# Kernel optimization log

Hardware: AMD Instinct MI355X
Metric: run time of the kernel (lower is better)

## Reference

```python
import jax, jax.numpy as jnp
import numpy as np
from jax import lax

B, T_ENCO, N_INP, N_HID, T_DECO = 1024, 128, 128, 256, 24


def _lin(x, W, b):
    return x @ W.T + b


def _lstm_cell(x, h, c, Wih, Whh, bih, bhh):
    # PyTorch LSTMCell gate order: input, forget, cell(g), output
    g = x @ Wih.T + bih + h @ Whh.T + bhh
    i, f, gg, o = jnp.split(g, 4, axis=-1)
    c2 = jax.nn.sigmoid(f) * c + jax.nn.sigmoid(i) * jnp.tanh(gg)
    return jax.nn.sigmoid(o) * jnp.tanh(c2), c2


def setup_inputs() -> dict:
    key = jax.random.key(0)
    ks = iter(jax.random.split(key, 48))
    def w(shape, s=0.05):
        return jax.random.normal(next(ks), shape, jnp.float32) * s
    m = N_HID
    return {
        "input_p_q": jax.random.normal(next(ks), (B, T_ENCO, N_INP), jnp.float32),
        "label_p": jax.random.normal(next(ks), (B, T_DECO), jnp.float32),
        "Ue_W": w((m, T_ENCO)), "Ue_b": w((m,)),
        "Ue2_W": w((m, N_INP)), "Ue2_b": w((m,)),
        "We_W": w((m, 2 * N_HID)), "We_b": w((m,)),
        "Ve_W": w((1, m)), "Ve_b": w((1,)),
        "Ud_W": w((N_HID, N_HID)), "Ud_b": w((N_HID,)),
        "Wd_W": w((N_HID, 2 * N_HID)), "Wd_b": w((N_HID,)),
        "Vd_W": w((1, N_HID)), "Vd_b": w((1,)),
        "enc_Wih": w((4 * N_HID, N_INP)), "enc_Whh": w((4 * N_HID, N_HID)),
        "enc_bih": w((4 * N_HID,)), "enc_bhh": w((4 * N_HID,)),
        "mid_Wih": w((4 * N_HID, N_HID)), "mid_Whh": w((4 * N_HID, N_HID)),
        "mid_bih": w((4 * N_HID,)), "mid_bhh": w((4 * N_HID,)),
        "dec_Wih": w((4 * N_HID, N_HID)), "dec_Whh": w((4 * N_HID, N_HID)),
        "dec_bih": w((4 * N_HID,)), "dec_bhh": w((4 * N_HID,)),
        "reg_W": w((1, N_HID)), "reg_b": w((1,)),
    }


def reference(input_p_q, label_p, Ue_W, Ue_b, Ue2_W, Ue2_b, We_W, We_b, Ve_W, Ve_b,
              Ud_W, Ud_b, Wd_W, Wd_b, Vd_W, Vd_b,
              enc_Wih, enc_Whh, enc_bih, enc_bhh,
              mid_Wih, mid_Whh, mid_bih, mid_bhh,
              dec_Wih, dec_Whh, dec_bih, dec_bhh,
              reg_W, reg_b):
    bsz = input_p_q.shape[0]
    inputs = input_p_q[:, :T_ENCO, :]                       # [B, T, n_inp]
    # Ue(inputs.transpose(1,2)) is loop-invariant: [B, n_inp, m]
    ue_x = _lin(jnp.swapaxes(inputs, 1, 2), Ue_W, Ue_b)
    z = jnp.zeros((bsz, N_HID), inputs.dtype)

    # --- spatial-attention encoder (LSTMCell over time) ---
    def enc_step(carry, x_i):                               # x_i: [B, n_inp]
        h, c = carry
        hc = _lin(jnp.concatenate([h, c], axis=1), We_W, We_b)[:, None, :]
        xi = _lin(x_i, Ue2_W, Ue2_b)[:, None, :]
        score = _lin(jnp.tanh(hc + ue_x + xi), Ve_W, Ve_b)[..., 0]  # [B, n_inp]
        a = jax.nn.softmax(score, axis=1)
        h2, c2 = _lstm_cell(x_i * a, h, c, enc_Wih, enc_Whh, enc_bih, enc_bhh)
        return (h2, c2), h2

    _, enc_hs = lax.scan(enc_step, (z, z), jnp.swapaxes(inputs, 0, 1))  # [T, B, H]

    # --- middle single-layer LSTM (zero init state) ---
    def mid_step(carry, x_t):
        h, c = carry
        h2, c2 = _lstm_cell(x_t, h, c, mid_Wih, mid_Whh, mid_bih, mid_bhh)
        return (h2, c2), h2

    _, mid = lax.scan(mid_step, (z, z), enc_hs)
    mid = jnp.swapaxes(mid, 0, 1)                            # [B, T, H]
    ud_mid = _lin(mid, Ud_W, Ud_b)                           # loop-invariant

    # --- temporal-attention decoder (note: raw (un-softmaxed) scores used in bmm,
    #     matching the original code) ---
    def dec_step(carry, _):
        hi, ci = carry
        wd = _lin(jnp.concatenate([hi, ci], axis=1), Wd_W, Wd_b)[:, None, :]
        t = _lin(jnp.tanh(wd + ud_mid), Vd_W, Vd_b)[..., 0]  # [B, T]
        dec_in = jnp.einsum('bt,bth->bh', t, mid)
        hi2, ci2 = _lstm_cell(dec_in, hi, ci, dec_Wih, dec_Whh, dec_bih, dec_bhh)
        return (hi2, ci2), hi2

    _, dec = lax.scan(dec_step, (z, z), None, length=T_DECO + 6)
    dec = jnp.swapaxes(dec, 0, 1)                            # [B, T_deco+6, H]
    out = _lin(dec, reg_W, reg_b)[..., 0]                    # [B, T_deco+6]
    return out[:, -T_DECO:]
```

## Files before the change

kernel.cpp:

```cpp
#include <hip/hip_runtime.h>


#define B_   1024
#define T_   128
#define NI_  128
#define H_   256
#define H4_  1024
#define TD_  24
#define DS_  30
#define BB   4
#define TB   1024

typedef _Float16 hf_t;
typedef _Float16 half8  __attribute__((ext_vector_type(8)));
typedef _Float16 half2v __attribute__((ext_vector_type(2)));

__device__ __forceinline__ float sigm(float x) {
    return __builtin_amdgcn_rcpf(1.0f + __expf(-x));
}
__device__ __forceinline__ float tanh_f(float x) {
    float e = __expf(2.0f * x);
    return 1.0f - 2.0f * __builtin_amdgcn_rcpf(e + 1.0f);
}
__device__ __forceinline__ float fdot2f(half2v a, half2v b, float c) {
#if __has_builtin(__builtin_amdgcn_fdot2)
    return __builtin_amdgcn_fdot2(a, b, c, false);
#else
    return fmaf((float)a.x, (float)b.x, fmaf((float)a.y, (float)b.y, c));
#endif
}
__device__ __forceinline__ float dot8h(half8 w, half8 x, float acc) {
    acc = fdot2f(__builtin_shufflevector(w, w, 0, 1), __builtin_shufflevector(x, x, 0, 1), acc);
    acc = fdot2f(__builtin_shufflevector(w, w, 2, 3), __builtin_shufflevector(x, x, 2, 3), acc);
    acc = fdot2f(__builtin_shufflevector(w, w, 4, 5), __builtin_shufflevector(x, x, 4, 5), acc);
    acc = fdot2f(__builtin_shufflevector(w, w, 6, 7), __builtin_shufflevector(x, x, 6, 7), acc);
    return acc;
}
__device__ __forceinline__ hf_t nt_load_h(const hf_t* p) {
#if __has_builtin(__builtin_nontemporal_load)
    return __builtin_nontemporal_load(p);
#else
    return *p;
#endif
}
__device__ __forceinline__ void nt_store_h(hf_t v, hf_t* p) {
#if __has_builtin(__builtin_nontemporal_store)
    __builtin_nontemporal_store(v, p);
#else
    *p = v;
#endif
}

#define W_WE    0u
#define W_UE2   131072u
#define W_EWIH  163840u
#define W_EWHH  294912u
#define W_MWIH  557056u
#define W_MWHH  819200u
#define W_DWIH  1081344u
#define W_DWHH  1343488u
#define W_WD    1605632u
#define W_UD    1736704u
#define SCR_A   2097152u
#define SCR_B   35651584u

__global__ void convw_kernel(const float* __restrict__ sWE, const float* __restrict__ sUE2,
                             const float* __restrict__ sEI, const float* __restrict__ sEH,
                             const float* __restrict__ sMI, const float* __restrict__ sMH,
                             const float* __restrict__ sDI, const float* __restrict__ sDH,
                             const float* __restrict__ sWD, const float* __restrict__ sUD,
                             hf_t* __restrict__ dst) {
    const int gtid = blockIdx.x * blockDim.x + threadIdx.x;
    const int gs   = gridDim.x * blockDim.x;
    for (int n = gtid; n < 131072; n += gs) {
        int e = n & 7, q = n >> 3, k = q & 255, c = q >> 8, kq = c >> 4, i = c & 15;
        dst[W_WE + n] = (hf_t)sWE[k * 512 + kq * 128 + i * 8 + e];
    }
    for (int n = gtid; n < 32768; n += gs) {
        int e = n & 7, q = n >> 3, k = q & 255, c = q >> 8, kq = c >> 2, i = c & 3;
        dst[W_UE2 + n] = (hf_t)sUE2[k * 128 + kq * 32 + i * 8 + e];
    }
    for (int n = gtid; n < 131072; n += gs) {
        int e = n & 7, q = n >> 3, o = q & 1023, i = q >> 10;
        dst[W_EWIH + n] = (hf_t)sEI[o * 128 + i * 8 + e];
    }
    for (int n = gtid; n < 262144; n += gs) {
        int e = n & 7, q = n >> 3, o = q & 1023, i = q >> 10;
        int s = o * 256 + i * 8 + e;
        dst[W_EWHH + n] = (hf_t)sEH[s];
        dst[W_MWIH + n] = (hf_t)sMI[s];
        dst[W_MWHH + n] = (hf_t)sMH[s];
        dst[W_DWIH + n] = (hf_t)sDI[s];
        dst[W_DWHH + n] = (hf_t)sDH[s];
    }
    for (int n = gtid; n < 131072; n += gs) {
        int e = n & 7, q = n >> 3, k = q & 255, c = q >> 8, kq = c >> 4, i = c & 15;
        dst[W_WD + n] = (hf_t)sWD[k * 512 + kq * 128 + i * 8 + e];
    }
    for (int n = gtid; n < 65536; n += gs)
        dst[W_UD + n] = (hf_t)sUD[n];
}

#define O_HC    0
#define O_CF    1024
#define O_HM    2048
#define O_CMF   2560
#define O_XRAW  3584
#define O_XH    4096
#define O_XG    4352
#define O_HCXI  4608
#define O_SPART 5632
#define O_SBUF  6656
#define O_GBUF  7168
#define O_DINH  11264
#define O_HF    11776
#define O_VES   12800
#define O_VDS   13056

__global__ __launch_bounds__(TB, 4) void dsrnn_kernel(
    const float* __restrict__ inp,
    const float* __restrict__ UeW,  const float* __restrict__ Ueb,
    const float* __restrict__ Ue2b,
    const float* __restrict__ Web,
    const float* __restrict__ VeW,  const float* __restrict__ Veb,
    const float* __restrict__ Udb,
    const float* __restrict__ Wdb,
    const float* __restrict__ VdW,  const float* __restrict__ Vdb,
    const float* __restrict__ ebih, const float* __restrict__ ebhh,
    const float* __restrict__ mbih, const float* __restrict__ mbhh,
    const float* __restrict__ dbih, const float* __restrict__ dbhh,
    const float* __restrict__ rW,   const float* __restrict__ rb,
    const hf_t* __restrict__ wb,
    hf_t* __restrict__ scrA,
    hf_t* __restrict__ scrB,
    float* __restrict__ out)
{
    __shared__ float sm[16384];
    const int tid = threadIdx.x;
    const int b0  = blockIdx.x * BB;

    hf_t*  hc   = (hf_t*)(sm + O_HC);
    float* cf   = sm + O_CF;
    hf_t*  hm   = (hf_t*)(sm + O_HM);
    float* cmf  = sm + O_CMF;
    float* xraw = sm + O_XRAW;
    hf_t*  xh   = (hf_t*)(sm + O_XH);
    hf_t*  xg   = (hf_t*)(sm + O_XG);
    float* hcxi = sm + O_HCXI;
    float* spart= sm + O_SPART;
    float* sbuf = sm + O_SBUF;
    float* gbuf = sm + O_GBUF;
    hf_t*  dinh = (hf_t*)(sm + O_DINH);
    float* hful = sm + O_HF;
    float* ves  = sm + O_VES;
    float* vds  = sm + O_VDS;

    {
        const int j = tid & 127, kq8 = tid >> 7;
        for (int b = 0; b < BB; ++b) {
            __syncthreads();
            const float* Xg = inp + (size_t)(b0 + b) * T_ * NI_;
            for (int i = tid; i < T_ * NI_; i += TB) sm[i] = Xg[i];
            __syncthreads();
            hf_t* ub = scrA + (size_t)(b0 + b) * H_ * NI_;
            for (int k = kq8 * 32; k < kq8 * 32 + 32; ++k) {
                const float* wrow = UeW + (size_t)k * T_;
                float acc = Ueb[k];
#pragma unroll 4
                for (int t = 0; t < T_; ++t) acc = fmaf(wrow[t], sm[t * NI_ + j], acc);
                nt_store_h((hf_t)acc, ub + (size_t)k * NI_ + j);
            }
        }
    }
    __syncthreads();
    for (int i = tid; i < 3584; i += TB) sm[i] = 0.0f;
    if (tid < 256) { ves[tid] = VeW[tid]; vds[tid] = VdW[tid]; }
    __syncthreads();

    for (int t = 0; t < T_; ++t) {
        if (tid < 512) {
            const int b = tid >> 7, j = tid & 127;
            float v = inp[((size_t)(b0 + b) * T_ + t) * NI_ + j];
            xraw[b * NI_ + j] = v;
            xh[b * NI_ + j]   = (hf_t)v;
        }
        __syncthreads();

        {
            const int k = tid & 255, kq = tid >> 8;
            const half8* wWE = (const half8*)(wb + W_WE)  + (size_t)(kq * 16) * 256 + k;
            const half8* wU2 = (const half8*)(wb + W_UE2) + (size_t)(kq * 4)  * 256 + k;
            float a0 = 0.f, a1 = 0.f, a2 = 0.f, a3 = 0.f;
#pragma unroll 8
            for (int i = 0; i < 16; ++i) {
                half8 w = wWE[(size_t)i * 256];
                a0 = dot8h(w, *(const half8*)&hc[0 * 512 + kq * 128 + i * 8], a0);
                a1 = dot8h(w, *(const half8*)&hc[1 * 512 + kq * 128 + i * 8], a1);
                a2 = dot8h(w, *(const half8*)&hc[2 * 512 + kq * 128 + i * 8], a2);
                a3 = dot8h(w, *(const half8*)&hc[3 * 512 + kq * 128 + i * 8], a3);
            }
#pragma unroll
            for (int i = 0; i < 4; ++i) {
                half8 w = wU2[(size_t)i * 256];
                a0 = dot8h(w, *(const half8*)&xh[0 * 128 + kq * 32 + i * 8], a0);
                a1 = dot8h(w, *(const half8*)&xh[1 * 128 + kq * 32 + i * 8], a1);
                a2 = dot8h(w, *(const half8*)&xh[2 * 128 + kq * 32 + i * 8], a2);
                a3 = dot8h(w, *(const half8*)&xh[3 * 128 + kq * 32 + i * 8], a3);
            }
            gbuf[kq * 1024 + 0 * 256 + k] = a0;
            gbuf[kq * 1024 + 1 * 256 + k] = a1;
            gbuf[kq * 1024 + 2 * 256 + k] = a2;
            gbuf[kq * 1024 + 3 * 256 + k] = a3;
        }
        __syncthreads();
        {
            const int b = tid >> 8, k = tid & 255;
            hcxi[b * 256 + k] = gbuf[b * 256 + k] + gbuf[1024 + b * 256 + k]
                              + gbuf[2048 + b * 256 + k] + gbuf[3072 + b * 256 + k]
                              + Web[k] + Ue2b[k];
        }
        __syncthreads();

        {
            const int b = tid >> 8, r = tid & 255, kh = r >> 7, j = r & 127;
            const hf_t* up = scrA + ((size_t)(b0 + b) * 256 + kh * 128) * 128 + j;
            const float* hx = hcxi + b * 256 + kh * 128;
            const float* vw = ves + kh * 128;
            float acc = kh ? 0.f : Veb[0];
#pragma unroll 8
            for (int k2 = 0; k2 < 128; ++k2) {
                float u = (float)nt_load_h(up + (size_t)k2 * 128);
                acc = fmaf(vw[k2], tanh_f(hx[k2] + u), acc);
            }
            spart[tid] = acc;
        }
        __syncthreads();

        if (tid < 256) {
            const int b = tid >> 6, lane = tid & 63;
            const int base = b << 8;
            float sA = spart[base + lane]      + spart[base + 128 + lane];
            float sB = spart[base + 64 + lane] + spart[base + 192 + lane];
            float m = fmaxf(sA, sB);
            for (int d = 1; d < 64; d <<= 1) m = fmaxf(m, __shfl_xor(m, d));
            float eA = __expf(sA - m), eB = __expf(sB - m);
            float ssum = eA + eB;
            for (int d = 1; d < 64; d <<= 1) ssum += __shfl_xor(ssum, d);
            float inv = 1.0f / ssum;
            xg[b * NI_ + lane]      = (hf_t)(xraw[b * NI_ + lane] * eA * inv);
            xg[b * NI_ + lane + 64] = (hf_t)(xraw[b * NI_ + lane + 64] * eB * inv);
        }
        __syncthreads();

        {
            const int o = tid;
            const half8* wih = (const half8*)(wb + W_EWIH) + o;
            const half8* whh = (const half8*)(wb + W_EWHH) + o;
            float bias = ebih[o] + ebhh[o];
            float a0 = bias, a1 = bias, a2 = bias, a3 = bias;
#pragma unroll 8
            for (int i = 0; i < 16; ++i) {
                half8 w = wih[(size_t)i * 1024];
                a0 = dot8h(w, *(const half8*)&xg[0 * 128 + i * 8], a0);
                a1 = dot8h(w, *(const half8*)&xg[1 * 128 + i * 8], a1);
                a2 = dot8h(w, *(const half8*)&xg[2 * 128 + i * 8], a2);
                a3 = dot8h(w, *(const half8*)&xg[3 * 128 + i * 8], a3);
            }
#pragma unroll 8
            for (int i = 0; i < 32; ++i) {
                half8 w = whh[(size_t)i * 1024];
                a0 = dot8h(w, *(const half8*)&hc[0 * 512 + i * 8], a0);
                a1 = dot8h(w, *(const half8*)&hc[1 * 512 + i * 8], a1);
                a2 = dot8h(w, *(const half8*)&hc[2 * 512 + i * 8], a2);
                a3 = dot8h(w, *(const half8*)&hc[3 * 512 + i * 8], a3);
            }
            gbuf[0 * 1024 + o] = a0; gbuf[1 * 1024 + o] = a1;
            gbuf[2 * 1024 + o] = a2; gbuf[3 * 1024 + o] = a3;
        }
        __syncthreads();

        {
            const int b = tid >> 8, k = tid & 255;
            float gi = gbuf[b * H4_ + k];
            float gf = gbuf[b * H4_ + H_ + k];
            float gg = gbuf[b * H4_ + 2 * H_ + k];
            float go = gbuf[b * H4_ + 3 * H_ + k];
            float c2 = sigm(gf) * cf[b * H_ + k] + sigm(gi) * tanh_f(gg);
            float h2 = sigm(go) * tanh_f(c2);
            cf[b * H_ + k] = c2;
            hc[b * 512 + k]       = (hf_t)h2;
            hc[b * 512 + 256 + k] = (hf_t)c2;
        }
        __syncthreads();

        {
            const int o = tid;
            const half8* wih = (const half8*)(wb + W_MWIH) + o;
            const half8* whh = (const half8*)(wb + W_MWHH) + o;
            float bias = mbih[o] + mbhh[o];
            float a0 = bias, a1 = bias, a2 = bias, a3 = bias;
#pragma unroll 8
            for (int i = 0; i < 32; ++i) {
                half8 w = wih[(size_t)i * 1024];
                a0 = dot8h(w, *(const half8*)&hc[0 * 512 + i * 8], a0);
                a1 = dot8h(w, *(const half8*)&hc[1 * 512 + i * 8], a1);
                a2 = dot8h(w, *(const half8*)&hc[2 * 512 + i * 8], a2);
                a3 = dot8h(w, *(const half8*)&hc[3 * 512 + i * 8], a3);
            }
#pragma unroll 8
            for (int i = 0; i < 32; ++i) {
                half8 w = whh[(size_t)i * 1024];
                a0 = dot8h(w, *(const half8*)&hm[0 * 256 + i * 8], a0);
                a1 = dot8h(w, *(const half8*)&hm[1 * 256 + i * 8], a1);
                a2 = dot8h(w, *(const half8*)&hm[2 * 256 + i * 8], a2);
                a3 = dot8h(w, *(const half8*)&hm[3 * 256 + i * 8], a3);
            }
            gbuf[0 * 1024 + o] = a0; gbuf[1 * 1024 + o] = a1;
            gbuf[2 * 1024 + o] = a2; gbuf[3 * 1024 + o] = a3;
        }
        __syncthreads();

        {
            const int b = tid >> 8, k = tid & 255;
            float gi = gbuf[b * H4_ + k];
            float gf = gbuf[b * H4_ + H_ + k];
            float gg = gbuf[b * H4_ + 2 * H_ + k];
            float go = gbuf[b * H4_ + 3 * H_ + k];
            float c2 = sigm(gf) * cmf[b * H_ + k] + sigm(gi) * tanh_f(gg);
            float h2 = sigm(go) * tanh_f(c2);
            cmf[b * H_ + k] = c2;
            hm[b * 256 + k] = (hf_t)h2;
            scrB[((size_t)(b0 + b) * T_ + t) * H_ + k] = (hf_t)h2;
        }
        __syncthreads();
    }

    {
        const int b = tid >> 8, r = tid & 255, oh = r >> 7, tt = r & 127;
        const half8* mrow = (const half8*)(scrB + ((size_t)(b0 + b) * T_ + tt) * H_);
        half8 m[32];
#pragma unroll
        for (int i = 0; i < 32; ++i) m[i] = mrow[i];
        const half8* udw = (const half8*)(wb + W_UD);
        for (int o2 = 0; o2 < 128; ++o2) {
            const int o = oh * 128 + o2;
            const half8* ur = udw + (size_t)o * 32;
            float acc = Udb[o];
#pragma unroll 8
            for (int i = 0; i < 32; ++i) acc = dot8h(ur[i], m[i], acc);
            nt_store_h((hf_t)acc, scrA + ((size_t)(b0 + b) * 256 + o) * 128 + tt);
        }
    }
    __syncthreads();
    for (int i = tid; i < 2048; i += TB) sm[i] = 0.0f;
    __syncthreads();

    for (int s = 0; s < DS_; ++s) {
        {
            const int k = tid & 255, kq = tid >> 8;
            const half8* wWD = (const half8*)(wb + W_WD) + (size_t)(kq * 16) * 256 + k;
            float a0 = 0.f, a1 = 0.f, a2 = 0.f, a3 = 0.f;
#pragma unroll 8
            for (int i = 0; i < 16; ++i) {
                half8 w = wWD[(size_t)i * 256];
                a0 = dot8h(w, *(const half8*)&hc[0 * 512 + kq * 128 + i * 8], a0);
                a1 = dot8h(w, *(const half8*)&hc[1 * 512 + kq * 128 + i * 8], a1);
                a2 = dot8h(w, *(const half8*)&hc[2 * 512 + kq * 128 + i * 8], a2);
                a3 = dot8h(w, *(const half8*)&hc[3 * 512 + kq * 128 + i * 8], a3);
            }
            gbuf[kq * 1024 + 0 * 256 + k] = a0;
            gbuf[kq * 1024 + 1 * 256 + k] = a1;
            gbuf[kq * 1024 + 2 * 256 + k] = a2;
            gbuf[kq * 1024 + 3 * 256 + k] = a3;
        }
        __syncthreads();
        {
            const int b = tid >> 8, k = tid & 255;
            hcxi[b * 256 + k] = gbuf[b * 256 + k] + gbuf[1024 + b * 256 + k]
                              + gbuf[2048 + b * 256 + k] + gbuf[3072 + b * 256 + k]
                              + Wdb[k];
        }
        __syncthreads();

        {
            const int b = tid >> 8, r = tid & 255, kh = r >> 7, j = r & 127;
            const hf_t* up = scrA + ((size_t)(b0 + b) * 256 + kh * 128) * 128 + j;
            const float* hx = hcxi + b * 256 + kh * 128;
            const float* vw = vds + kh * 128;
            float acc = kh ? 0.f : Vdb[0];
#pragma unroll 8
            for (int k2 = 0; k2 < 128; ++k2) {
                float u = (float)nt_load_h(up + (size_t)k2 * 128);
                acc = fmaf(vw[k2], tanh_f(hx[k2] + u), acc);
            }
            spart[tid] = acc;
        }
        __syncthreads();
        if (tid < 512) {
            const int b = tid >> 7, j = tid & 127;
            sbuf[b * T_ + j] = spart[(b << 8) + j] + spart[(b << 8) + 128 + j];
        }
        __syncthreads();

        {
            const int b = tid >> 8, h = tid & 255;
            const hf_t* mp = scrB + (size_t)(b0 + b) * T_ * H_ + h;
            float acc = 0.0f;
            for (int j = 0; j < T_; ++j)
                acc = fmaf(sbuf[b * T_ + j], (float)mp[(size_t)j * H_], acc);
            dinh[b * 256 + h] = (hf_t)acc;
        }
        __syncthreads();

        {
            const int o = tid;
            const half8* wih = (const half8*)(wb + W_DWIH) + o;
            const half8* whh = (const half8*)(wb + W_DWHH) + o;
            float bias = dbih[o] + dbhh[o];
            float a0 = bias, a1 = bias, a2 = bias, a3 = bias;
#pragma unroll 8
            for (int i = 0; i < 32; ++i) {
                half8 w = wih[(size_t)i * 1024];
                a0 = dot8h(w, *(const half8*)&dinh[0 * 256 + i * 8], a0);
                a1 = dot8h(w, *(const half8*)&dinh[1 * 256 + i * 8], a1);
                a2 = dot8h(w, *(const half8*)&dinh[2 * 256 + i * 8], a2);
                a3 = dot8h(w, *(const half8*)&dinh[3 * 256 + i * 8], a3);
            }
#pragma unroll 8
            for (int i = 0; i < 32; ++i) {
                half8 w = whh[(size_t)i * 1024];
                a0 = dot8h(w, *(const half8*)&hc[0 * 512 + i * 8], a0);
                a1 = dot8h(w, *(const half8*)&hc[1 * 512 + i * 8], a1);
                a2 = dot8h(w, *(const half8*)&hc[2 * 512 + i * 8], a2);
                a3 = dot8h(w, *(const half8*)&hc[3 * 512 + i * 8], a3);
            }
            gbuf[0 * 1024 + o] = a0; gbuf[1 * 1024 + o] = a1;
            gbuf[2 * 1024 + o] = a2; gbuf[3 * 1024 + o] = a3;
        }
        __syncthreads();

        {
            const int b = tid >> 8, k = tid & 255;
            float gi = gbuf[b * H4_ + k];
            float gf = gbuf[b * H4_ + H_ + k];
            float gg = gbuf[b * H4_ + 2 * H_ + k];
            float go = gbuf[b * H4_ + 3 * H_ + k];
            float c2 = sigm(gf) * cf[b * H_ + k] + sigm(gi) * tanh_f(gg);
            float h2 = sigm(go) * tanh_f(c2);
            cf[b * H_ + k] = c2;
            hc[b * 512 + k]       = (hf_t)h2;
            hc[b * 512 + 256 + k] = (hf_t)c2;
            hful[b * H_ + k] = h2;
        }
        __syncthreads();

        if (s >= 6 && tid < 256) {
            const int b = tid >> 6, lane = tid & 63;
            float p = rW[lane]       * hful[b * H_ + lane]
                    + rW[lane + 64]  * hful[b * H_ + lane + 64]
                    + rW[lane + 128] * hful[b * H_ + lane + 128]
                    + rW[lane + 192] * hful[b * H_ + lane + 192];
            for (int d = 1; d < 64; d <<= 1) p += __shfl_xor(p, d);
            if (lane == 0) out[(size_t)(b0 + b) * TD_ + (s - 6)] = p + rb[0];
        }
        __syncthreads();
    }
}

extern "C" void kernel_launch(void* const* d_in, const int* in_sizes, int n_in,
                              void* d_out, int out_size, void* d_ws, size_t ws_size,
                              hipStream_t stream) {
    const float* inp  = (const float*)d_in[0];
    const float* UeW  = (const float*)d_in[2];
    const float* Ueb  = (const float*)d_in[3];
    const float* Ue2W = (const float*)d_in[4];
    const float* Ue2b = (const float*)d_in[5];
    const float* WeW  = (const float*)d_in[6];
    const float* Web  = (const float*)d_in[7];
    const float* VeW  = (const float*)d_in[8];
    const float* Veb  = (const float*)d_in[9];
    const float* UdW  = (const float*)d_in[10];
    const float* Udb  = (const float*)d_in[11];
    const float* WdW  = (const float*)d_in[12];
    const float* Wdb  = (const float*)d_in[13];
    const float* VdW  = (const float*)d_in[14];
    const float* Vdb  = (const float*)d_in[15];
    const float* eWih = (const float*)d_in[16];
    const float* eWhh = (const float*)d_in[17];
    const float* ebih = (const float*)d_in[18];
    const float* ebhh = (const float*)d_in[19];
    const float* mWih = (const float*)d_in[20];
    const float* mWhh = (const float*)d_in[21];
    const float* mbih = (const float*)d_in[22];
    const float* mbhh = (const float*)d_in[23];
    const float* dWih = (const float*)d_in[24];
    const float* dWhh = (const float*)d_in[25];
    const float* dbih = (const float*)d_in[26];
    const float* dbhh = (const float*)d_in[27];
    const float* rW   = (const float*)d_in[28];
    const float* rb   = (const float*)d_in[29];

    hf_t* wsb  = (hf_t*)d_ws;
    hf_t* scrA = wsb + SCR_A;
    hf_t* scrB = wsb + SCR_B;

    convw_kernel<<<512, 256, 0, stream>>>(WeW, Ue2W, eWih, eWhh, mWih, mWhh,
                                          dWih, dWhh, WdW, UdW, wsb);

    dsrnn_kernel<<<B_ / BB, TB, 0, stream>>>(
        inp, UeW, Ueb, Ue2b, Web, VeW, Veb, Udb, Wdb, VdW, Vdb,
        ebih, ebhh, mbih, mbhh, dbih, dbhh, rW, rb,
        wsb, scrA, scrB, (float*)d_out);
}
```

Measured before the change: 10.76 ms.

## Use tanh addition identity, transpose attention scratch, split LSTM gate GEMVs

New measurement: 11.06 ms. 1.03x slower.

```diff
diff --git a/kernel.cpp b/kernel.cpp
--- a/kernel.cpp
+++ b/kernel.cpp
@@ -36,20 +36,6 @@
     acc = fdot2f(__builtin_shufflevector(w, w, 6, 7), __builtin_shufflevector(x, x, 6, 7), acc);
     return acc;
 }
-__device__ __forceinline__ hf_t nt_load_h(const hf_t* p) {
-#if __has_builtin(__builtin_nontemporal_load)
-    return __builtin_nontemporal_load(p);
-#else
-    return *p;
-#endif
-}
-__device__ __forceinline__ void nt_store_h(hf_t v, hf_t* p) {
-#if __has_builtin(__builtin_nontemporal_store)
-    __builtin_nontemporal_store(v, p);
-#else
-    *p = v;
-#endif
-}
 
 #define W_WE    0u
 #define W_UE2   131072u
@@ -108,14 +94,13 @@
 #define O_XRAW  3584
 #define O_XH    4096
 #define O_XG    4352
-#define O_HCXI  4608
+#define O_TA    4608
 #define O_SPART 5632
 #define O_SBUF  6656
-#define O_GBUF  7168
-#define O_DINH  11264
-#define O_HF    11776
-#define O_VES   12800
-#define O_VDS   13056
+#define O_DINH  7168
+#define O_VES   7680
+#define O_VDS   7936
+#define O_GBUF  8192
 
 __global__ __launch_bounds__(TB, 4) void dsrnn_kernel(
     const float* __restrict__ inp,
@@ -146,14 +131,14 @@
     float* xraw = sm + O_XRAW;
     hf_t*  xh   = (hf_t*)(sm + O_XH);
     hf_t*  xg   = (hf_t*)(sm + O_XG);
-    float* hcxi = sm + O_HCXI;
+    float* TaB  = sm + O_TA;
     float* spart= sm + O_SPART;
     float* sbuf = sm + O_SBUF;
-    float* gbuf = sm + O_GBUF;
     hf_t*  dinh = (hf_t*)(sm + O_DINH);
-    float* hful = sm + O_HF;
+    float* hful = sm + O_SPART;
     float* ves  = sm + O_VES;
     float* vds  = sm + O_VDS;
+    float* gbuf = sm + O_GBUF;
 
     {
         const int j = tid & 127, kq8 = tid >> 7;
@@ -162,13 +147,18 @@
             const float* Xg = inp + (size_t)(b0 + b) * T_ * NI_;
             for (int i = tid; i < T_ * NI_; i += TB) sm[i] = Xg[i];
             __syncthreads();
-            hf_t* ub = scrA + (size_t)(b0 + b) * H_ * NI_;
-            for (int k = kq8 * 32; k < kq8 * 32 + 32; ++k) {
-                const float* wrow = UeW + (size_t)k * T_;
-                float acc = Ueb[k];
+            hf_t* ub = scrA + (size_t)(b0 + b) * NI_ * H_;
+            for (int k0 = kq8 * 32; k0 < kq8 * 32 + 32; k0 += 8) {
+                half8 v;
+#pragma unroll
+                for (int kk = 0; kk < 8; ++kk) {
+                    const float* wrow = UeW + (size_t)(k0 + kk) * T_;
+                    float acc = Ueb[k0 + kk];
 #pragma unroll 4
-                for (int t = 0; t < T_; ++t) acc = fmaf(wrow[t], sm[t * NI_ + j], acc);
-                nt_store_h((hf_t)acc, ub + (size_t)k * NI_ + j);
+                    for (int t = 0; t < T_; ++t) acc = fmaf(wrow[t], sm[t * NI_ + j], acc);
+                    v[kk] = (hf_t)tanh_f(acc);
+                }
+                *(half8*)&ub[(size_t)j * H_ + k0] = v;
             }
         }
     }
@@ -215,22 +205,35 @@
         __syncthreads();
         {
             const int b = tid >> 8, k = tid & 255;
-            hcxi[b * 256 + k] = gbuf[b * 256 + k] + gbuf[1024 + b * 256 + k]
-                              + gbuf[2048 + b * 256 + k] + gbuf[3072 + b * 256 + k]
-                              + Web[k] + Ue2b[k];
+            float s = gbuf[b * 256 + k] + gbuf[1024 + b * 256 + k]
+                    + gbuf[2048 + b * 256 + k] + gbuf[3072 + b * 256 + k]
+                    + Web[k] + Ue2b[k];
+            TaB[b * 256 + k] = tanh_f(s);
         }
         __syncthreads();
 
         {
             const int b = tid >> 8, r = tid & 255, kh = r >> 7, j = r & 127;
-            const hf_t* up = scrA + ((size_t)(b0 + b) * 256 + kh * 128) * 128 + j;
-            const float* hx = hcxi + b * 256 + kh * 128;
+            const half8* up = (const half8*)(scrA + ((size_t)(b0 + b) * NI_ + j) * H_ + kh * 128);
+            const float* ta = TaB + b * 256 + kh * 128;
             const float* vw = ves + kh * 128;
             float acc = kh ? 0.f : Veb[0];
-#pragma unroll 8
-            for (int k2 = 0; k2 < 128; ++k2) {
-                float u = (float)nt_load_h(up + (size_t)k2 * 128);
-                acc = fmaf(vw[k2], tanh_f(hx[k2] + u), acc);
+#pragma unroll 4
+            for (int i = 0; i < 16; ++i) {
+                half8 u = up[i];
+                float4 t0 = *(const float4*)&ta[i * 8];
+                float4 t1 = *(const float4*)&ta[i * 8 + 4];
+                float4 v0 = *(const float4*)&vw[i * 8];
+                float4 v1 = *(const float4*)&vw[i * 8 + 4];
+                const float tt[8] = {t0.x, t0.y, t0.z, t0.w, t1.x, t1.y, t1.z, t1.w};
+                const float vv[8] = {v0.x, v0.y, v0.z, v0.w, v1.x, v1.y, v1.z, v1.w};
+#pragma unroll
+                for (int e = 0; e < 8; ++e) {
+                    float tu  = (float)u[e];
+                    float num = tt[e] + tu;
+                    float den = fmaf(tt[e], tu, 1.0f);
+                    acc = fmaf(vv[e] * num, __builtin_amdgcn_rcpf(den), acc);
+                }
             }
             spart[tid] = acc;
         }
@@ -253,38 +256,73 @@
         __syncthreads();
 
         {
-            const int o = tid;
-            const half8* wih = (const half8*)(wb + W_EWIH) + o;
-            const half8* whh = (const half8*)(wb + W_EWHH) + o;
-            float bias = ebih[o] + ebhh[o];
-            float a0 = bias, a1 = bias, a2 = bias, a3 = bias;
-#pragma unroll 8
-            for (int i = 0; i < 16; ++i) {
-                half8 w = wih[(size_t)i * 1024];
-                a0 = dot8h(w, *(const half8*)&xg[0 * 128 + i * 8], a0);
-                a1 = dot8h(w, *(const half8*)&xg[1 * 128 + i * 8], a1);
-                a2 = dot8h(w, *(const half8*)&xg[2 * 128 + i * 8], a2);
-                a3 = dot8h(w, *(const half8*)&xg[3 * 128 + i * 8], a3);
-            }
-#pragma unroll 8
-            for (int i = 0; i < 32; ++i) {
-                half8 w = whh[(size_t)i * 1024];
-                a0 = dot8h(w, *(const half8*)&hc[0 * 512 + i * 8], a0);
-                a1 = dot8h(w, *(const half8*)&hc[1 * 512 + i * 8], a1);
-                a2 = dot8h(w, *(const half8*)&hc[2 * 512 + i * 8], a2);
-                a3 = dot8h(w, *(const half8*)&hc[3 * 512 + i * 8], a3);
-            }
-            gbuf[0 * 1024 + o] = a0; gbuf[1 * 1024 + o] = a1;
-            gbuf[2 * 1024 + o] = a2; gbuf[3 * 1024 + o] = a3;
+            const int op = tid & 511, kq = tid >> 9;
+            float a00, a01, a02, a03, a10, a11, a12, a13;
+            if (kq == 0) {
+                float b0v = ebih[op] + ebhh[op];
+                float b1v = ebih[op + 512] + ebhh[op + 512];
+                a00 = a01 = a02 = a03 = b0v;
+                a10 = a11 = a12 = a13 = b1v;
+                const half8* wiA = (const half8*)(wb + W_EWIH) + op;
+                const half8* wiB = (const half8*)(wb + W_EWIH) + op + 512;
+#pragma unroll 8
+                for (int i = 0; i < 16; ++i) {
+                    half8 w0 = wiA[(size_t)i * 1024], w1 = wiB[(size_t)i * 1024];
+                    half8 x0 = *(const half8*)&xg[0 * 128 + i * 8];
+                    half8 x1 = *(const half8*)&xg[1 * 128 + i * 8];
+                    half8 x2 = *(const half8*)&xg[2 * 128 + i * 8];
+                    half8 x3 = *(const half8*)&xg[3 * 128 + i * 8];
+                    a00 = dot8h(w0, x0, a00); a01 = dot8h(w0, x1, a01);
+                    a02 = dot8h(w0, x2, a02); a03 = dot8h(w0, x3, a03);
+                    a10 = dot8h(w1, x0, a10); a11 = dot8h(w1, x1, a11);
+                    a12 = dot8h(w1, x2, a12); a13 = dot8h(w1, x3, a13);
+                }
+                const half8* whA = (const half8*)(wb + W_EWHH) + op;
+                const half8* whB = (const half8*)(wb + W_EWHH) + op + 512;
+#pragma unroll 8
+                for (int i = 0; i < 8; ++i) {
+                    half8 w0 = whA[(size_t)i * 1024], w1 = whB[(size_t)i * 1024];
+                    half8 h0v = *(const half8*)&hc[0 * 512 + i * 8];
+                    half8 h1v = *(const half8*)&hc[1 * 512 + i * 8];
+                    half8 h2v = *(const half8*)&hc[2 * 512 + i * 8];
+                    half8 h3v = *(const half8*)&hc[3 * 512 + i * 8];
+                    a00 = dot8h(w0, h0v, a00); a01 = dot8h(w0, h1v, a01);
+                    a02 = dot8h(w0, h2v, a02); a03 = dot8h(w0, h3v, a03);
+                    a10 = dot8h(w1, h0v, a10); a11 = dot8h(w1, h1v, a11);
+                    a12 = dot8h(w1, h2v, a12); a13 = dot8h(w1, h3v, a13);
+                }
+            } else {
+                a00 = a01 = a02 = a03 = 0.f;
+                a10 = a11 = a12 = a13 = 0.f;
+                const half8* whA = (const half8*)(wb + W_EWHH) + op;
+                const half8* whB = (const half8*)(wb + W_EWHH) + op + 512;
+#pragma unroll 8
+                for (int i = 8; i < 32; ++i) {
+                    half8 w0 = whA[(size_t)i * 1024], w1 = whB[(size_t)i * 1024];
+                    half8 h0v = *(const half8*)&hc[0 * 512 + i * 8];
+                    half8 h1v = *(const half8*)&hc[1 * 512 + i * 8];
+                    half8 h2v = *(const half8*)&hc[2 * 512 + i * 8];
+                    half8 h3v = *(const half8*)&hc[3 * 512 + i * 8];
+                    a00 = dot8h(w0, h0v, a00); a01 = dot8h(w0, h1v, a01);
+                    a02 = dot8h(w0, h2v, a02); a03 = dot8h(w0, h3v, a03);
+                    a10 = dot8h(w1, h0v, a10); a11 = dot8h(w1, h1v, a11);
+                    a12 = dot8h(w1, h2v, a12); a13 = dot8h(w1, h3v, a13);
+                }
+            }
+            float* gp = gbuf + kq * 4096;
+            gp[0 * 1024 + op] = a00; gp[1 * 1024 + op] = a01;
+            gp[2 * 1024 + op] = a02; gp[3 * 1024 + op] = a03;
+            gp[0 * 1024 + op + 512] = a10; gp[1 * 1024 + op + 512] = a11;
+            gp[2 * 1024 + op + 512] = a12; gp[3 * 1024 + op + 512] = a13;
         }
         __syncthreads();
 
         {
             const int b = tid >> 8, k = tid & 255;
-            float gi = gbuf[b * H4_ + k];
-            float gf = gbuf[b * H4_ + H_ + k];
-            float gg = gbuf[b * H4_ + 2 * H_ + k];
-            float go = gbuf[b * H4_ + 3 * H_ + k];
+            float gi = gbuf[b * H4_ + k]            + gbuf[4096 + b * H4_ + k];
+            float gf = gbuf[b * H4_ + H_ + k]       + gbuf[4096 + b * H4_ + H_ + k];
+            float gg = gbuf[b * H4_ + 2 * H_ + k]   + gbuf[4096 + b * H4_ + 2 * H_ + k];
+            float go = gbuf[b * H4_ + 3 * H_ + k]   + gbuf[4096 + b * H4_ + 3 * H_ + k];
             float c2 = sigm(gf) * cf[b * H_ + k] + sigm(gi) * tanh_f(gg);
             float h2 = sigm(go) * tanh_f(c2);
             cf[b * H_ + k] = c2;
@@ -294,38 +332,59 @@
         __syncthreads();
 
         {
-            const int o = tid;
-            const half8* wih = (const half8*)(wb + W_MWIH) + o;
-            const half8* whh = (const half8*)(wb + W_MWHH) + o;
-            float bias = mbih[o] + mbhh[o];
-            float a0 = bias, a1 = bias, a2 = bias, a3 = bias;
-#pragma unroll 8
-            for (int i = 0; i < 32; ++i) {
-                half8 w = wih[(size_t)i * 1024];
-                a0 = dot8h(w, *(const half8*)&hc[0 * 512 + i * 8], a0);
-                a1 = dot8h(w, *(const half8*)&hc[1 * 512 + i * 8], a1);
-                a2 = dot8h(w, *(const half8*)&hc[2 * 512 + i * 8], a2);
-                a3 = dot8h(w, *(const half8*)&hc[3 * 512 + i * 8], a3);
-            }
-#pragma unroll 8
-            for (int i = 0; i < 32; ++i) {
-                half8 w = whh[(size_t)i * 1024];
-                a0 = dot8h(w, *(const half8*)&hm[0 * 256 + i * 8], a0);
-                a1 = dot8h(w, *(const half8*)&hm[1 * 256 + i * 8], a1);
-                a2 = dot8h(w, *(const half8*)&hm[2 * 256 + i * 8], a2);
-                a3 = dot8h(w, *(const half8*)&hm[3 * 256 + i * 8], a3);
-            }
-            gbuf[0 * 1024 + o] = a0; gbuf[1 * 1024 + o] = a1;
-            gbuf[2 * 1024 + o] = a2; gbuf[3 * 1024 + o] = a3;
+            const int op = tid & 511, kq = tid >> 9;
+            float a00, a01, a02, a03, a10, a11, a12, a13;
+            if (kq == 0) {
+                float b0v = mbih[op] + mbhh[op];
+                float b1v = mbih[op + 512] + mbhh[op + 512];
+                a00 = a01 = a02 = a03 = b0v;
+                a10 = a11 = a12 = a13 = b1v;
+                const half8* wA = (const half8*)(wb + W_MWIH) + op;
+                const half8* wB = (const half8*)(wb + W_MWIH) + op + 512;
+#pragma unroll 8
+                for (int i = 0; i < 32; ++i) {
+                    half8 w0 = wA[(size_t)i * 1024], w1 = wB[(size_t)i * 1024];
+                    half8 h0v = *(const half8*)&hc[0 * 512 + i * 8];
+                    half8 h1v = *(const half8*)&hc[1 * 512 + i * 8];
+                    half8 h2v = *(const half8*)&hc[2 * 512 + i * 8];
+                    half8 h3v = *(const half8*)&hc[3 * 512 + i * 8];
+                    a00 = dot8h(w0, h0v, a00); a01 = dot8h(w0, h1v, a01);
+                    a02 = dot8h(w0, h2v, a02); a03 = dot8h(w0, h3v, a03);
+                    a10 = dot8h(w1, h0v, a10); a11 = dot8h(w1, h1v, a11);
+                    a12 = dot8h(w1, h2v, a12); a13 = dot8h(w1, h3v, a13);
+                }
+            } else {
+                a00 = a01 = a02 = a03 = 0.f;
+                a10 = a11 = a12 = a13 = 0.f;
+                const half8* wA = (const half8*)(wb + W_MWHH) + op;
+                const half8* wB = (const half8*)(wb + W_MWHH) + op + 512;
+#pragma unroll 8
+                for (int i = 0; i < 32; ++i) {
+                    half8 w0 = wA[(size_t)i * 1024], w1 = wB[(size_t)i * 1024];
+                    half8 h0v = *(const half8*)&hm[0 * 256 + i * 8];
+                    half8 h1v = *(const half8*)&hm[1 * 256 + i * 8];
+                    half8 h2v = *(const half8*)&hm[2 * 256 + i * 8];
+                    half8 h3v = *(const half8*)&hm[3 * 256 + i * 8];
+                    a00 = dot8h(w0, h0v, a00); a01 = dot8h(w0, h1v, a01);
+                    a02 = dot8h(w0, h2v, a02); a03 = dot8h(w0, h3v, a03);
+                    a10 = dot8h(w1, h0v, a10); a11 = dot8h(w1, h1v, a11);
+                    a12 = dot8h(w1, h2v, a12); a13 = dot8h(w1, h3v, a13);
+                }
+            }
+            float* gp = gbuf + kq * 4096;
+            gp[0 * 1024 + op] = a00; gp[1 * 1024 + op] = a01;
+            gp[2 * 1024 + op] = a02; gp[3 * 1024 + op] = a03;
+            gp[0 * 1024 + op + 512] = a10; gp[1 * 1024 + op + 512] = a11;
+            gp[2 * 1024 + op + 512] = a12; gp[3 * 1024 + op + 512] = a13;
         }
         __syncthreads();
 
         {
             const int b = tid >> 8, k = tid & 255;
-            float gi = gbuf[b * H4_ + k];
-            float gf = gbuf[b * H4_ + H_ + k];
-            float gg = gbuf[b * H4_ + 2 * H_ + k];
-            float go = gbuf[b * H4_ + 3 * H_ + k];
+            float gi = gbuf[b * H4_ + k]            + gbuf[4096 + b * H4_ + k];
+            float gf = gbuf[b * H4_ + H_ + k]       + gbuf[4096 + b * H4_ + H_ + k];
+            float gg = gbuf[b * H4_ + 2 * H_ + k]   + gbuf[4096 + b * H4_ + 2 * H_ + k];
+            float go = gbuf[b * H4_ + 3 * H_ + k]   + gbuf[4096 + b * H4_ + 3 * H_ + k];
             float c2 = sigm(gf) * cmf[b * H_ + k] + sigm(gi) * tanh_f(gg);
             float h2 = sigm(go) * tanh_f(c2);
             cmf[b * H_ + k] = c2;
@@ -342,13 +401,17 @@
 #pragma unroll
         for (int i = 0; i < 32; ++i) m[i] = mrow[i];
         const half8* udw = (const half8*)(wb + W_UD);
-        for (int o2 = 0; o2 < 128; ++o2) {
-            const int o = oh * 128 + o2;
-            const half8* ur = udw + (size_t)o * 32;
-            float acc = Udb[o];
-#pragma unroll 8
-            for (int i = 0; i < 32; ++i) acc = dot8h(ur[i], m[i], acc);
-            nt_store_h((hf_t)acc, scrA + ((size_t)(b0 + b) * 256 + o) * 128 + tt);
+        for (int o0 = oh * 128; o0 < oh * 128 + 128; o0 += 8) {
+            half8 v;
+#pragma unroll
+            for (int oo = 0; oo < 8; ++oo) {
+                const half8* ur = udw + (size_t)(o0 + oo) * 32;
+                float acc = Udb[o0 + oo];
+#pragma unroll 8
+                for (int i = 0; i < 32; ++i) acc = dot8h(ur[i], m[i], acc);
+                v[oo] = (hf_t)tanh_f(acc);
+            }
+            *(half8*)&scrA[((size_t)(b0 + b) * T_ + tt) * H_ + o0] = v;
         }
     }
     __syncthreads();
@@ -376,22 +439,35 @@
         __syncthreads();
         {
             const int b = tid >> 8, k = tid & 255;
-            hcxi[b * 256 + k] = gbuf[b * 256 + k] + gbuf[1024 + b * 256 + k]
-                              + gbuf[2048 + b * 256 + k] + gbuf[3072 + b * 256 + k]
-                              + Wdb[k];
+            float sv = gbuf[b * 256 + k] + gbuf[1024 + b * 256 + k]
+                     + gbuf[2048 + b * 256 + k] + gbuf[3072 + b * 256 + k]
+                     + Wdb[k];
+            TaB[b * 256 + k] = tanh_f(sv);
         }
         __syncthreads();
 
         {
             const int b = tid >> 8, r = tid & 255, kh = r >> 7, j = r & 127;
-            const hf_t* up = scrA + ((size_t)(b0 + b) * 256 + kh * 128) * 128 + j;
-            const float* hx = hcxi + b * 256 + kh * 128;
+            const half8* up = (const half8*)(scrA + ((size_t)(b0 + b) * T_ + j) * H_ + kh * 128);
+            const float* ta = TaB + b * 256 + kh * 128;
             const float* vw = vds + kh * 128;
             float acc = kh ? 0.f : Vdb[0];
-#pragma unroll 8
-            for (int k2 = 0; k2 < 128; ++k2) {
-                float u = (float)nt_load_h(up + (size_t)k2 * 128);
-                acc = fmaf(vw[k2], tanh_f(hx[k2] + u), acc);
+#pragma unroll 4
+            for (int i = 0; i < 16; ++i) {
+                half8 u = up[i];
+                float4 t0 = *(const float4*)&ta[i * 8];
+                float4 t1 = *(const float4*)&ta[i * 8 + 4];
+                float4 v0 = *(const float4*)&vw[i * 8];
+                float4 v1 = *(const float4*)&vw[i * 8 + 4];
+                const float tt[8] = {t0.x, t0.y, t0.z, t0.w, t1.x, t1.y, t1.z, t1.w};
+                const float vv[8] = {v0.x, v0.y, v0.z, v0.w, v1.x, v1.y, v1.z, v1.w};
+#pragma unroll
+                for (int e = 0; e < 8; ++e) {
+                    float tu  = (float)u[e];
+                    float num = tt[e] + tu;
+                    float den = fmaf(tt[e], tu, 1.0f);
+                    acc = fmaf(vv[e] * num, __builtin_amdgcn_rcpf(den), acc);
+                }
             }
             spart[tid] = acc;
         }
@@ -413,38 +489,59 @@
         __syncthreads();
 
         {
-            const int o = tid;
-            const half8* wih = (const half8*)(wb + W_DWIH) + o;
-            const half8* whh = (const half8*)(wb + W_DWHH) + o;
-            float bias = dbih[o] + dbhh[o];
-            float a0 = bias, a1 = bias, a2 = bias, a3 = bias;
-#pragma unroll 8
-            for (int i = 0; i < 32; ++i) {
-                half8 w = wih[(size_t)i * 1024];
-                a0 = dot8h(w, *(const half8*)&dinh[0 * 256 + i * 8], a0);
-                a1 = dot8h(w, *(const half8*)&dinh[1 * 256 + i * 8], a1);
-                a2 = dot8h(w, *(const half8*)&dinh[2 * 256 + i * 8], a2);
-                a3 = dot8h(w, *(const half8*)&dinh[3 * 256 + i * 8], a3);
-            }
-#pragma unroll 8
-            for (int i = 0; i < 32; ++i) {
-                half8 w = whh[(size_t)i * 1024];
-                a0 = dot8h(w, *(const half8*)&hc[0 * 512 + i * 8], a0);
-                a1 = dot8h(w, *(const half8*)&hc[1 * 512 + i * 8], a1);
-                a2 = dot8h(w, *(const half8*)&hc[2 * 512 + i * 8], a2);
-                a3 = dot8h(w, *(const half8*)&hc[3 * 512 + i * 8], a3);
-            }
-            gbuf[0 * 1024 + o] = a0; gbuf[1 * 1024 + o] = a1;
-            gbuf[2 * 1024 + o] = a2; gbuf[3 * 1024 + o] = a3;
+            const int op = tid & 511, kq = tid >> 9;
+            float a00, a01, a02, a03, a10, a11, a12, a13;
+            if (kq == 0) {
+                float b0v = dbih[op] + dbhh[op];
+                float b1v = dbih[op + 512] + dbhh[op + 512];
+                a00 = a01 = a02 = a03 = b0v;
+                a10 = a11 = a12 = a13 = b1v;
+                const half8* wA = (const half8*)(wb + W_DWIH) + op;
+                const half8* wB = (const half8*)(wb + W_DWIH) + op + 512;
+#pragma unroll 8
+                for (int i = 0; i < 32; ++i) {
+                    half8 w0 = wA[(size_t)i * 1024], w1 = wB[(size_t)i * 1024];
+                    half8 x0 = *(const half8*)&dinh[0 * 256 + i * 8];
+                    half8 x1 = *(const half8*)&dinh[1 * 256 + i * 8];
+                    half8 x2 = *(const half8*)&dinh[2 * 256 + i * 8];
+                    half8 x3 = *(const half8*)&dinh[3 * 256 + i * 8];
+                    a00 = dot8h(w0, x0, a00); a01 = dot8h(w0, x1, a01);
+                    a02 = dot8h(w0, x2, a02); a03 = dot8h(w0, x3, a03);
+                    a10 = dot8h(w1, x0, a10); a11 = dot8h(w1, x1, a11);
+                    a12 = dot8h(w1, x2, a12); a13 = dot8h(w1, x3, a13);
+                }
+            } else {
+                a00 = a01 = a02 = a03 = 0.f;
+                a10 = a11 = a12 = a13 = 0.f;
+                const half8* wA = (const half8*)(wb + W_DWHH) + op;
+                const half8* wB = (const half8*)(wb + W_DWHH) + op + 512;
+#pragma unroll 8
+                for (int i = 0; i < 32; ++i) {
+                    half8 w0 = wA[(size_t)i * 1024], w1 = wB[(size_t)i * 1024];
+                    half8 h0v = *(const half8*)&hc[0 * 512 + i * 8];
+                    half8 h1v = *(const half8*)&hc[1 * 512 + i * 8];
+                    half8 h2v = *(const half8*)&hc[2 * 512 + i * 8];
+                    half8 h3v = *(const half8*)&hc[3 * 512 + i * 8];
+                    a00 = dot8h(w0, h0v, a00); a01 = dot8h(w0, h1v, a01);
+                    a02 = dot8h(w0, h2v, a02); a03 = dot8h(w0, h3v, a03);
+                    a10 = dot8h(w1, h0v, a10); a11 = dot8h(w1, h1v, a11);
+                    a12 = dot8h(w1, h2v, a12); a13 = dot8h(w1, h3v, a13);
+                }
+            }
+            float* gp = gbuf + kq * 4096;
+            gp[0 * 1024 + op] = a00; gp[1 * 1024 + op] = a01;
+            gp[2 * 1024 + op] = a02; gp[3 * 1024 + op] = a03;
+            gp[0 * 1024 + op + 512] = a10; gp[1 * 1024 + op + 512] = a11;
+            gp[2 * 1024 + op + 512] = a12; gp[3 * 1024 + op + 512] = a13;
         }
         __syncthreads();
 
         {
             const int b = tid >> 8, k = tid & 255;
-            float gi = gbuf[b * H4_ + k];
-            float gf = gbuf[b * H4_ + H_ + k];
-            float gg = gbuf[b * H4_ + 2 * H_ + k];
-            float go = gbuf[b * H4_ + 3 * H_ + k];
+            float gi = gbuf[b * H4_ + k]            + gbuf[4096 + b * H4_ + k];
+            float gf = gbuf[b * H4_ + H_ + k]       + gbuf[4096 + b * H4_ + H_ + k];
+            float gg = gbuf[b * H4_ + 2 * H_ + k]   + gbuf[4096 + b * H4_ + 2 * H_ + k];
+            float go = gbuf[b * H4_ + 3 * H_ + k]   + gbuf[4096 + b * H4_ + 3 * H_ + k];
             float c2 = sigm(gf) * cf[b * H_ + k] + sigm(gi) * tanh_f(gg);
             float h2 = sigm(go) * tanh_f(c2);
             cf[b * H_ + k] = c2;
```
